# Optimization experiments

Measured on AMD Instinct MI355X. Metric: run time of the kernel, lower is better.

## Reference

```python
import jax, jax.numpy as jnp
import numpy as np


def setup_inputs() -> dict:
    key = jax.random.key(0)
    k0, k1, k2, k3, k4 = jax.random.split(key, 5)
    B, H, W, C = 8, 64, 64, 256
    d = C // 8
    scale = 0.02
    return {
        "inputs": jax.random.normal(k0, (B, H, W, C), dtype=jnp.float32),
        "w_q": jax.random.normal(k1, (C, d), dtype=jnp.float32) * scale,
        "w_k": jax.random.normal(k2, (C, d), dtype=jnp.float32) * scale,
        "w_v": jax.random.normal(k3, (C, C), dtype=jnp.float32) * scale,
        "w_out": jax.random.normal(k4, (C, C), dtype=jnp.float32) * scale,
    }


def reference(inputs, w_q, w_k, w_v, w_out):
    B, H, W, C = inputs.shape
    N = H * W
    x = inputs.reshape(B, N, C)  # 1x1 conv == per-pixel channel matmul
    q = jnp.einsum("bnc,cd->bnd", x, w_q)   # [B, N, C//8]
    k = jnp.einsum("bnc,cd->bnd", x, w_k)   # [B, N, C//8]
    v = jnp.einsum("bnc,ce->bne", x, w_v)   # [B, N, C]
    attn = jax.nn.softmax(jnp.einsum("bnd,bmd->bnm", q, k), axis=-1)  # [B, N, N]
    attended = jnp.einsum("bnm,bme->bne", attn, v)  # [B, N, C]
    out = jnp.einsum("bne,ec->bnc", attended, w_out)
    return inputs + out.reshape(B, H, W, C)
```

## Files before the change

kernel.cpp:

```cpp
#include <hip/hip_runtime.h>
#include <hip/hip_bf16.h>
#include <stdint.h>

typedef __attribute__((ext_vector_type(8))) short short8;
typedef __attribute__((ext_vector_type(8))) unsigned short ushort8;
typedef __attribute__((ext_vector_type(4))) unsigned short ushort4v;
typedef __attribute__((ext_vector_type(4))) unsigned u32x4;
typedef __attribute__((ext_vector_type(2))) float f32x2;
typedef __attribute__((ext_vector_type(4))) float f32x4;
typedef __attribute__((ext_vector_type(16))) float f32x16;

#define B_ 8
#define N_ 4096
#define C_ 256
#define D_ 32
#define LOG2E 1.44269504088896f

__device__ inline unsigned short f2bf(float f) {
  union { float f; unsigned u; } v; v.f = f;
  unsigned r = v.u + 0x7fffu + ((v.u >> 16) & 1u);
  return (unsigned short)(r >> 16);
}
__device__ inline float bf2f(unsigned short u) {
  return __uint_as_float(((unsigned)u) << 16);
}
__device__ inline float exp2_fast(float x) {
  float r; asm("v_exp_f32 %0, %1" : "=v"(r) : "v"(x)); return r;
}
__device__ inline unsigned cvt_pk_bf16(float lo, float hi) {
  unsigned r; asm("v_cvt_pk_bf16_f32 %0, %1, %2" : "=v"(r) : "v"(lo), "v"(hi)); return r;
}
__device__ inline void permlane32_swap(unsigned& a, unsigned& b) {
  asm volatile("v_permlane32_swap_b32 %0, %1" : "+v"(a), "+v"(b));
}
__device__ inline void gll16(const unsigned short* src, void* lds) {
  __builtin_amdgcn_global_load_lds((const __attribute__((address_space(1))) void*)src,
                                   (__attribute__((address_space(3))) void*)lds, 16, 0, 0);
}

__device__ inline size_t wf_addr(int C, int kk) {
  int ct = C >> 4, cl = C & 15, s = kk >> 5, gf = (kk >> 3) & 3, j = kk & 7;
  return ((size_t)((ct * 8 + s) * 64 + gf * 16 + cl)) * 8 + j;
}

__global__ __launch_bounds__(256) void prep_kernel(const float* __restrict__ wq,
                                                   const float* __restrict__ wk,
                                                   const float* __restrict__ wo,
                                                   const float* __restrict__ wv,
                                                   unsigned short* __restrict__ wf,
                                                   unsigned short* __restrict__ wv_b,
                                                   unsigned short* __restrict__ woT_b) {
  int i = blockIdx.x * 256 + threadIdx.x;
  if (i < 16384) {
    int C = i >> 8, kk = i & 255;
    float v = (C < 32) ? wq[kk * 32 + C] * LOG2E : wk[kk * 32 + (C - 32)];
    wf[wf_addr(C, kk)] = f2bf(v);
  } else if (i < 81920) {
    int j = i - 16384;
    wv_b[j] = f2bf(wv[j]);
  } else {
    int j = i - 81920;
    int e2 = j >> 8, e = j & 255;
    woT_b[j] = f2bf(wo[e * 256 + e2]);
  }
}

__global__ __launch_bounds__(256) void prep2_kernel(const unsigned short* __restrict__ woT_b,
                                                    const unsigned short* __restrict__ wv_b,
                                                    unsigned short* __restrict__ wf) {
  const int lane = threadIdx.x & 63, w = threadIdx.x >> 6;
  const int g = lane >> 4, li = lane & 15;
  const int m0 = blockIdx.x * 64 + w * 16;
  const unsigned short* arow = woT_b + (size_t)(m0 + li) * 256 + (g << 3);
  const unsigned short* brow = wv_b + (size_t)li * 256 + (g << 3);
  f32x4 acc[16] = {};
  for (int kk = 0; kk < 256; kk += 32) {
    short8 a = *reinterpret_cast<const short8*>(arow + kk);
#pragma unroll
    for (int ct = 0; ct < 16; ++ct) {
      short8 bb = *reinterpret_cast<const short8*>(brow + (size_t)ct * 16 * 256 + kk);
      acc[ct] = __builtin_amdgcn_mfma_f32_16x16x32_bf16(a, bb, acc[ct], 0, 0, 0);
    }
  }
#pragma unroll
  for (int ct = 0; ct < 16; ++ct)
#pragma unroll
    for (int r = 0; r < 4; ++r) {
      const int C = 64 + m0 + (g << 2) + r;
      const int kk = ct * 16 + li;
      wf[wf_addr(C, kk)] = f2bf(acc[ct][r]);
    }
}

__global__ __launch_bounds__(256, 2) void qkv_kernel(const float* __restrict__ x,
                                                     const unsigned short* __restrict__ wf,
                                                     unsigned short* __restrict__ q,
                                                     unsigned short* __restrict__ k,
                                                     unsigned short* __restrict__ vwT) {
  __shared__ __align__(16) unsigned short xs[64 * 256];
  const int tid = threadIdx.x;
  const int l = tid & 63, w = tid >> 6;
  const int bx = blockIdx.x;
  const int g = l >> 4, li = l & 15;
  const int m0 = bx * 64;

  const unsigned short* wfb = wf + (size_t)(w * 5) * 4096;

  short8 BA[5], BB[5];
#pragma unroll
  for (int c = 0; c < 5; ++c)
    BA[c] = *reinterpret_cast<const short8*>(wfb + ((size_t)(c * 8 + 0) * 64 + l) * 8);
#pragma unroll
  for (int c = 0; c < 5; ++c)
    BB[c] = *reinterpret_cast<const short8*>(wfb + ((size_t)(c * 8 + 1) * 64 + l) * 8);

  {
    const int row = tid >> 2, qtr = tid & 3;
    const float* src = x + (size_t)(m0 + row) * 256 + qtr * 64;
    unsigned short* dstrow = xs + row * 256;
#pragma unroll
    for (int jj = 0; jj < 8; ++jj) {
      f32x4 a0 = *reinterpret_cast<const f32x4*>(src + jj * 8);
      f32x4 a1 = *reinterpret_cast<const f32x4*>(src + jj * 8 + 4);
      union { unsigned u[4]; ushort8 v; } P;
      P.u[0] = cvt_pk_bf16(a0[0], a0[1]); P.u[1] = cvt_pk_bf16(a0[2], a0[3]);
      P.u[2] = cvt_pk_bf16(a1[0], a1[1]); P.u[3] = cvt_pk_bf16(a1[2], a1[3]);
      const int blk = (qtr * 8 + jj) ^ (row & 7);
      *reinterpret_cast<ushort8*>(dstrow + blk * 8) = P.v;
    }
  }
  __syncthreads();

  f32x4 acc[4][5] = {};

#define QSTEP(S, BV, WN, PREF)                                                       \
  {                                                                                  \
    asm volatile("s_waitcnt vmcnt(" WN ")" ::: "memory");                            \
    __builtin_amdgcn_sched_barrier(0);                                               \
    short8 a_[4];                                                                    \
    _Pragma("unroll") for (int mt = 0; mt < 4; ++mt) {                               \
      const int row = mt * 16 + li;                                                  \
      a_[mt] = *reinterpret_cast<const short8*>(                                     \
          xs + row * 256 + ((((S) * 4 + g) ^ (row & 7)) << 3));                      \
    }                                                                                \
    _Pragma("unroll") for (int mt = 0; mt < 4; ++mt)                                 \
        _Pragma("unroll") for (int c = 0; c < 5; ++c)                                \
            acc[mt][c] = __builtin_amdgcn_mfma_f32_16x16x32_bf16(a_[mt], BV[c],      \
                                                                 acc[mt][c], 0, 0, 0); \
    if (PREF) {                                                                      \
      _Pragma("unroll") for (int c = 0; c < 5; ++c)                                  \
          BV[c] = *reinterpret_cast<const short8*>(                                  \
              wfb + ((size_t)(c * 8 + (S) + 2) * 64 + l) * 8);                       \
    }                                                                                \
  }

  QSTEP(0, BA, "5", true)
  QSTEP(1, BB, "5", true)
  QSTEP(2, BA, "5", true)
  QSTEP(3, BB, "5", true)
  QSTEP(4, BA, "5", true)
  QSTEP(5, BB, "5", true)
  QSTEP(6, BA, "5", false)
  QSTEP(7, BB, "0", false)
#undef QSTEP

  const int bb_ = bx >> 6;
#pragma unroll
  for (int mt = 0; mt < 4; ++mt) {
    const int nloc = (bx & 63) * 64 + mt * 16 + (g << 2);
#pragma unroll
    for (int c = 0; c < 5; ++c) {
      const int Cg = w * 5 + c;
      if (Cg < 2) {
        const int col = Cg * 16 + li;
#pragma unroll
        for (int r = 0; r < 4; ++r)
          q[((size_t)bb_ * N_ + nloc + r) * D_ + col] = f2bf(acc[mt][c][r]);
      } else if (Cg < 4) {
        const int col = (Cg - 2) * 16 + li;
#pragma unroll
        for (int r = 0; r < 4; ++r)
          k[((size_t)bb_ * N_ + nloc + r) * D_ + col] = f2bf(acc[mt][c][r]);
      } else {
        const int vc = Cg * 16 + li - 64;
        union { unsigned u[2]; ushort4v v; } P;
        P.u[0] = cvt_pk_bf16(acc[mt][c][0], acc[mt][c][1]);
        P.u[1] = cvt_pk_bf16(acc[mt][c][2], acc[mt][c][3]);
        *reinterpret_cast<ushort4v*>(&vwT[((size_t)bb_ * C_ + vc) * N_ + nloc]) = P.v;
      }
    }
  }
}

__global__ __launch_bounds__(512, 2) void flash_kernel(const unsigned short* __restrict__ q,
                                                       const unsigned short* __restrict__ k,
                                                       const unsigned short* __restrict__ vwT,
                                                       const float* __restrict__ x,
                                                       float* __restrict__ out) {
  __shared__ __align__(16) char smem[147456];
  const int tid = threadIdx.x;
  const int l = tid & 63, w_ = tid >> 6;
  const int kvh = w_ >> 2, qg = w_ & 3;
  const int blk = blockIdx.x;
  const int b = blk & 7;
  const int qt = blk >> 3;
  const int h = l >> 5, l31 = l & 31;
  const int R = kvh * 65536;

  const unsigned short* kb_ = k + (size_t)b * N_ * D_;
  const unsigned short* vb_ = vwT + (size_t)b * C_ * N_;

  const int qposb = qt * 128 + qg * 32;
  const size_t qoff = ((size_t)b * N_ + qposb + l31) * D_ + h * 8;
  const short8 qb0 = *reinterpret_cast<const short8*>(q + qoff);
  const short8 qb1 = *reinterpret_cast<const short8*>(q + qoff + 16);
  asm volatile("s_waitcnt vmcnt(0)" ::: "memory");

  const int vrow = l >> 3;
  const int vsrc = ((l & 7) ^ ((l >> 3) & 7)) << 3;
  const int krow = l >> 2;
  const int ksrc = ((l & 3) ^ ((l >> 3) & 3)) << 3;
  const int kvbase = kvh * 2048;

#define STAGE(BUF, KV0)                                                           \
  {                                                                               \
    char* vd = smem + R + (BUF) * 32768 + qg * 8192;                              \
    _Pragma("unroll") for (int t = 0; t < 8; ++t)                                 \
        gll16(vb_ + (size_t)(qg * 64 + t * 8 + vrow) * N_ + (KV0) + vsrc,         \
              vd + t * 1024);                                                     \
    gll16(kb_ + (size_t)((KV0) + qg * 16 + krow) * D_ + ksrc,                     \
          smem + 131072 + kvh * 8192 + (BUF) * 4096 + qg * 1024);                 \
  }

  f32x16 o[8] = {};
  float lsum = 0.f;
  const f32x16 z16 = {};
  const int kkey = (l31 >> 1) & 3;

  STAGE(0, kvbase)

  for (int i = 0; i < 32; ++i) {
    const int buf = i & 1;
    asm volatile("s_waitcnt vmcnt(0)" ::: "memory");
    __builtin_amdgcn_sched_barrier(0);
    __builtin_amdgcn_s_barrier();
    if (i < 31) STAGE(buf ^ 1, kvbase + (i + 1) * 64)
    const char* Vb = smem + R + buf * 32768;
    const char* Kb = smem + 131072 + kvh * 8192 + buf * 4096;
#pragma unroll
    for (int kvt = 0; kvt < 2; ++kvt) {
      const int krow32 = (kvt * 32 + l31) * 64;
      short8 ka0 = *reinterpret_cast<const short8*>(Kb + krow32 + (((0 + h) ^ kkey) << 4));
      short8 ka1 = *reinterpret_cast<const short8*>(Kb + krow32 + (((2 + h) ^ kkey) << 4));
      f32x16 s = __builtin_amdgcn_mfma_f32_32x32x16_bf16(ka0, qb0, z16, 0, 0, 0);
      s = __builtin_amdgcn_mfma_f32_32x32x16_bf16(ka1, qb1, s, 0, 0, 0);
#pragma unroll
      for (int r = 0; r < 16; ++r) s[r] = exp2_fast(s[r]);
      lsum += (((s[0] + s[1]) + (s[2] + s[3])) + ((s[4] + s[5]) + (s[6] + s[7]))) +
              (((s[8] + s[9]) + (s[10] + s[11])) + ((s[12] + s[13]) + (s[14] + s[15])));
      short8 pf0, pf1;
      {
        unsigned x0 = cvt_pk_bf16(s[0], s[1]),   y0 = cvt_pk_bf16(s[4], s[5]);
        unsigned x1 = cvt_pk_bf16(s[2], s[3]),   y1 = cvt_pk_bf16(s[6], s[7]);
        unsigned x2 = cvt_pk_bf16(s[8], s[9]),   y2 = cvt_pk_bf16(s[12], s[13]);
        unsigned x3 = cvt_pk_bf16(s[10], s[11]), y3 = cvt_pk_bf16(s[14], s[15]);
        permlane32_swap(x0, y0); permlane32_swap(x1, y1);
        permlane32_swap(x2, y2); permlane32_swap(x3, y3);
        union U { unsigned u[4]; short8 v; };
        U u0; u0.u[0] = x0; u0.u[1] = x1; u0.u[2] = y0; u0.u[3] = y1;
        U u1; u1.u[0] = x2; u1.u[1] = x3; u1.u[2] = y2; u1.u[3] = y3;
        pf0 = u0.v; pf1 = u1.v;
      }
      __builtin_amdgcn_s_setprio(1);
#pragma unroll
      for (int ct = 0; ct < 8; ++ct) {
        const int rl = ct * 32 + l31;
        const int vkey = rl & 7;
        const int rb = rl * 128;
        short8 va0 = *reinterpret_cast<const short8*>(Vb + rb + (((kvt * 4 + 0 + h) ^ vkey) << 4));
        short8 va1 = *reinterpret_cast<const short8*>(Vb + rb + (((kvt * 4 + 2 + h) ^ vkey) << 4));
        o[ct] = __builtin_amdgcn_mfma_f32_32x32x16_bf16(va0, pf0, o[ct], 0, 0, 0);
        o[ct] = __builtin_amdgcn_mfma_f32_32x32x16_bf16(va1, pf1, o[ct], 0, 0, 0);
      }
      __builtin_amdgcn_s_setprio(0);
    }
  }

  lsum += __shfl_xor(lsum, 32);
  __syncthreads();
  float* lb = reinterpret_cast<float*>(smem + 131072);
  if (h == 0) lb[kvh * 128 + qg * 32 + l31] = lsum;
  if (kvh == 1) {
    char* ob = smem + qg * 16384;
    int pg = 0;
#pragma unroll
    for (int ct = 0; ct < 8; ++ct)
#pragma unroll
      for (int jg = 0; jg < 2; ++jg) {
        u32x4 t;
#pragma unroll
        for (int e = 0; e < 4; ++e) {
          const int j = jg * 4 + e;
          t[e] = cvt_pk_bf16(o[ct][2 * j], o[ct][2 * j + 1]);
        }
        *reinterpret_cast<u32x4*>(ob + pg * 1024 + l * 16) = t;
        ++pg;
      }
  }
  __syncthreads();
  if (kvh == 0) {
    const float inv = 1.0f / (lb[qg * 32 + l31] + lb[128 + qg * 32 + l31]);
    const char* ob = smem + qg * 16384;
    int pg = 0;
#pragma unroll
    for (int ct = 0; ct < 8; ++ct)
#pragma unroll
      for (int jg = 0; jg < 2; ++jg) {
        u32x4 t = *reinterpret_cast<const u32x4*>(ob + pg * 1024 + l * 16);
        ++pg;
#pragma unroll
        for (int e = 0; e < 4; ++e) {
          const int j = jg * 4 + e;
          o[ct][2 * j]     += bf2f((unsigned short)(t[e] & 0xffffu));
          o[ct][2 * j + 1] += bf2f((unsigned short)(t[e] >> 16));
        }
      }
    const size_t rowbase = ((size_t)b * N_ + qposb + l31) * C_;
#pragma unroll
    for (int ct = 0; ct < 8; ++ct)
#pragma unroll
      for (int j = 0; j < 8; ++j) {
        const int c = ct * 32 + 2 * (j & 1) + 8 * (j >> 1) + 4 * h;
        f32x2 xr = *reinterpret_cast<const f32x2*>(x + rowbase + c);
        f32x2 t;
        t[0] = o[ct][2 * j] * inv + xr[0];
        t[1] = o[ct][2 * j + 1] * inv + xr[1];
        *reinterpret_cast<f32x2*>(out + rowbase + c) = t;
      }
  }
#undef STAGE
}

extern "C" void kernel_launch(void* const* d_in, const int* in_sizes, int n_in,
                              void* d_out, int out_size, void* d_ws, size_t ws_size,
                              hipStream_t stream) {
  const float* x  = (const float*)d_in[0];
  const float* wq = (const float*)d_in[1];
  const float* wk = (const float*)d_in[2];
  const float* wv = (const float*)d_in[3];
  const float* wo = (const float*)d_in[4];
  float* out = (float*)d_out;
  char* ws = (char*)d_ws;
  unsigned short* wf    = (unsigned short*)(ws + 0);
  unsigned short* wv_b  = (unsigned short*)(ws + 163840);
  unsigned short* woT_b = (unsigned short*)(ws + 294912);
  unsigned short* q     = (unsigned short*)(ws + 425984);
  unsigned short* k     = (unsigned short*)(ws + 2523136);
  unsigned short* vwT   = (unsigned short*)(ws + 4620288);

  prep_kernel<<<576, 256, 0, stream>>>(wq, wk, wo, wv, wf, wv_b, woT_b);
  prep2_kernel<<<4, 256, 0, stream>>>(woT_b, wv_b, wf);
  qkv_kernel<<<512, 256, 0, stream>>>(x, wf, q, k, vwT);
  flash_kernel<<<256, 512, 0, stream>>>(q, k, vwT, x, out);
}
```

Measured before the change: 125.4 us.

## Merge weight prep kernels and halve qkv tile to raise occupancy

Folds the two weight-preparation kernels into one launch: the Wo·Wv fused-weight MFMA now reads the fp32 weights directly and converts them to bf16 inline, so the intermediate bf16 buffers and one kernel launch go away. The qkv projection kernel switches to 32-row tiles with twice as many blocks and launch bounds of 3 blocks per CU. It also issues all x loads up front into registers before converting them and storing to LDS. The aim is to cut launch overhead and improve latency hiding in the projection stage. In exchange, the prep blocks do uncoalesced strided reads of Wo, and each weight fragment in the qkv kernel is reused across fewer rows.

Result: slower. 150.0 us (+19.6%).

```diff
diff --git a/kernel.cpp b/kernel.cpp
--- a/kernel.cpp
+++ b/kernel.cpp
@@ -47,65 +47,69 @@
                                                    const float* __restrict__ wk,
                                                    const float* __restrict__ wo,
                                                    const float* __restrict__ wv,
-                                                   unsigned short* __restrict__ wf,
-                                                   unsigned short* __restrict__ wv_b,
-                                                   unsigned short* __restrict__ woT_b) {
-  int i = blockIdx.x * 256 + threadIdx.x;
-  if (i < 16384) {
+                                                   unsigned short* __restrict__ wf) {
+  const int blk = blockIdx.x;
+  if (blk < 64) {
+    int i = blk * 256 + threadIdx.x;
     int C = i >> 8, kk = i & 255;
     float v = (C < 32) ? wq[kk * 32 + C] * LOG2E : wk[kk * 32 + (C - 32)];
     wf[wf_addr(C, kk)] = f2bf(v);
-  } else if (i < 81920) {
-    int j = i - 16384;
-    wv_b[j] = f2bf(wv[j]);
   } else {
-    int j = i - 81920;
-    int e2 = j >> 8, e = j & 255;
-    woT_b[j] = f2bf(wo[e * 256 + e2]);
-  }
-}
-
-__global__ __launch_bounds__(256) void prep2_kernel(const unsigned short* __restrict__ woT_b,
-                                                    const unsigned short* __restrict__ wv_b,
-                                                    unsigned short* __restrict__ wf) {
-  const int lane = threadIdx.x & 63, w = threadIdx.x >> 6;
-  const int g = lane >> 4, li = lane & 15;
-  const int m0 = blockIdx.x * 64 + w * 16;
-  const unsigned short* arow = woT_b + (size_t)(m0 + li) * 256 + (g << 3);
-  const unsigned short* brow = wv_b + (size_t)li * 256 + (g << 3);
-  f32x4 acc[16] = {};
-  for (int kk = 0; kk < 256; kk += 32) {
-    short8 a = *reinterpret_cast<const short8*>(arow + kk);
-#pragma unroll
-    for (int ct = 0; ct < 16; ++ct) {
-      short8 bb = *reinterpret_cast<const short8*>(brow + (size_t)ct * 16 * 256 + kk);
-      acc[ct] = __builtin_amdgcn_mfma_f32_16x16x32_bf16(a, bb, acc[ct], 0, 0, 0);
+    const int lane = threadIdx.x & 63, w = threadIdx.x >> 6;
+    const int g = lane >> 4, li = lane & 15;
+    const int m0 = (blk - 64) * 64 + w * 16;
+    f32x4 acc[16] = {};
+    for (int kk = 0; kk < 256; kk += 32) {
+      short8 a;
+#pragma unroll
+      for (int e = 0; e < 8; ++e)
+        a[e] = (short)f2bf(wo[(size_t)(kk + g * 8 + e) * 256 + (m0 + li)]);
+#pragma unroll
+      for (int ct = 0; ct < 16; ++ct) {
+        const float* bsrc = wv + (size_t)(ct * 16 + li) * 256 + kk + g * 8;
+        f32x4 b0 = *reinterpret_cast<const f32x4*>(bsrc);
+        f32x4 b1 = *reinterpret_cast<const f32x4*>(bsrc + 4);
+        union { unsigned u[4]; short8 v; } Bf;
+        Bf.u[0] = cvt_pk_bf16(b0[0], b0[1]); Bf.u[1] = cvt_pk_bf16(b0[2], b0[3]);
+        Bf.u[2] = cvt_pk_bf16(b1[0], b1[1]); Bf.u[3] = cvt_pk_bf16(b1[2], b1[3]);
+        acc[ct] = __builtin_amdgcn_mfma_f32_16x16x32_bf16(a, Bf.v, acc[ct], 0, 0, 0);
+      }
     }
-  }
-#pragma unroll
-  for (int ct = 0; ct < 16; ++ct)
-#pragma unroll
-    for (int r = 0; r < 4; ++r) {
-      const int C = 64 + m0 + (g << 2) + r;
-      const int kk = ct * 16 + li;
-      wf[wf_addr(C, kk)] = f2bf(acc[ct][r]);
-    }
-}
-
-__global__ __launch_bounds__(256, 2) void qkv_kernel(const float* __restrict__ x,
+#pragma unroll
+    for (int ct = 0; ct < 16; ++ct)
+#pragma unroll
+      for (int r = 0; r < 4; ++r) {
+        const int C = 64 + m0 + (g << 2) + r;
+        const int kk = ct * 16 + li;
+        wf[wf_addr(C, kk)] = f2bf(acc[ct][r]);
+      }
+  }
+}
+
+__global__ __launch_bounds__(256, 3) void qkv_kernel(const float* __restrict__ x,
                                                      const unsigned short* __restrict__ wf,
                                                      unsigned short* __restrict__ q,
                                                      unsigned short* __restrict__ k,
                                                      unsigned short* __restrict__ vwT) {
-  __shared__ __align__(16) unsigned short xs[64 * 256];
+  __shared__ __align__(16) unsigned short xs[32 * 256];
   const int tid = threadIdx.x;
   const int l = tid & 63, w = tid >> 6;
   const int bx = blockIdx.x;
   const int g = l >> 4, li = l & 15;
-  const int m0 = bx * 64;
+  const int m0 = bx * 32;
+
+  f32x4 xf[8];
+#pragma unroll
+  for (int r2 = 0; r2 < 4; ++r2) {
+    const int idx8 = r2 * 256 + tid;
+    const int row = idx8 >> 5, xb = idx8 & 31;
+    const float* src = x + (size_t)(m0 + row) * 256 + xb * 8;
+    xf[2 * r2]     = *reinterpret_cast<const f32x4*>(src);
+    xf[2 * r2 + 1] = *reinterpret_cast<const f32x4*>(src + 4);
+  }
+  __builtin_amdgcn_sched_barrier(0);
 
   const unsigned short* wfb = wf + (size_t)(w * 5) * 4096;
-
   short8 BA[5], BB[5];
 #pragma unroll
   for (int c = 0; c < 5; ++c)
@@ -114,36 +118,32 @@
   for (int c = 0; c < 5; ++c)
     BB[c] = *reinterpret_cast<const short8*>(wfb + ((size_t)(c * 8 + 1) * 64 + l) * 8);
 
-  {
-    const int row = tid >> 2, qtr = tid & 3;
-    const float* src = x + (size_t)(m0 + row) * 256 + qtr * 64;
-    unsigned short* dstrow = xs + row * 256;
-#pragma unroll
-    for (int jj = 0; jj < 8; ++jj) {
-      f32x4 a0 = *reinterpret_cast<const f32x4*>(src + jj * 8);
-      f32x4 a1 = *reinterpret_cast<const f32x4*>(src + jj * 8 + 4);
-      union { unsigned u[4]; ushort8 v; } P;
-      P.u[0] = cvt_pk_bf16(a0[0], a0[1]); P.u[1] = cvt_pk_bf16(a0[2], a0[3]);
-      P.u[2] = cvt_pk_bf16(a1[0], a1[1]); P.u[3] = cvt_pk_bf16(a1[2], a1[3]);
-      const int blk = (qtr * 8 + jj) ^ (row & 7);
-      *reinterpret_cast<ushort8*>(dstrow + blk * 8) = P.v;
-    }
+#pragma unroll
+  for (int r2 = 0; r2 < 4; ++r2) {
+    const int idx8 = r2 * 256 + tid;
+    const int row = idx8 >> 5, xb = idx8 & 31;
+    union { unsigned u[4]; ushort8 v; } P;
+    P.u[0] = cvt_pk_bf16(xf[2 * r2][0], xf[2 * r2][1]);
+    P.u[1] = cvt_pk_bf16(xf[2 * r2][2], xf[2 * r2][3]);
+    P.u[2] = cvt_pk_bf16(xf[2 * r2 + 1][0], xf[2 * r2 + 1][1]);
+    P.u[3] = cvt_pk_bf16(xf[2 * r2 + 1][2], xf[2 * r2 + 1][3]);
+    *reinterpret_cast<ushort8*>(&xs[row * 256 + ((xb ^ (row & 7)) << 3)]) = P.v;
   }
   __syncthreads();
 
-  f32x4 acc[4][5] = {};
+  f32x4 acc[2][5] = {};
 
 #define QSTEP(S, BV, WN, PREF)                                                       \
   {                                                                                  \
     asm volatile("s_waitcnt vmcnt(" WN ")" ::: "memory");                            \
     __builtin_amdgcn_sched_barrier(0);                                               \
-    short8 a_[4];                                                                    \
-    _Pragma("unroll") for (int mt = 0; mt < 4; ++mt) {                               \
+    short8 a_[2];                                                                    \
+    _Pragma("unroll") for (int mt = 0; mt < 2; ++mt) {                               \
       const int row = mt * 16 + li;                                                  \
       a_[mt] = *reinterpret_cast<const short8*>(                                     \
           xs + row * 256 + ((((S) * 4 + g) ^ (row & 7)) << 3));                      \
     }                                                                                \
-    _Pragma("unroll") for (int mt = 0; mt < 4; ++mt)                                 \
+    _Pragma("unroll") for (int mt = 0; mt < 2; ++mt)                                 \
         _Pragma("unroll") for (int c = 0; c < 5; ++c)                                \
             acc[mt][c] = __builtin_amdgcn_mfma_f32_16x16x32_bf16(a_[mt], BV[c],      \
                                                                  acc[mt][c], 0, 0, 0); \
@@ -164,10 +164,10 @@
   QSTEP(7, BB, "0", false)
 #undef QSTEP
 
-  const int bb_ = bx >> 6;
-#pragma unroll
-  for (int mt = 0; mt < 4; ++mt) {
-    const int nloc = (bx & 63) * 64 + mt * 16 + (g << 2);
+  const int bb_ = bx >> 7;
+#pragma unroll
+  for (int mt = 0; mt < 2; ++mt) {
+    const int nloc = (bx & 127) * 32 + mt * 16 + (g << 2);
 #pragma unroll
     for (int c = 0; c < 5; ++c) {
       const int Cg = w * 5 + c;
@@ -351,15 +351,12 @@
   const float* wo = (const float*)d_in[4];
   float* out = (float*)d_out;
   char* ws = (char*)d_ws;
-  unsigned short* wf    = (unsigned short*)(ws + 0);
-  unsigned short* wv_b  = (unsigned short*)(ws + 163840);
-  unsigned short* woT_b = (unsigned short*)(ws + 294912);
-  unsigned short* q     = (unsigned short*)(ws + 425984);
-  unsigned short* k     = (unsigned short*)(ws + 2523136);
-  unsigned short* vwT   = (unsigned short*)(ws + 4620288);
-
-  prep_kernel<<<576, 256, 0, stream>>>(wq, wk, wo, wv, wf, wv_b, woT_b);
-  prep2_kernel<<<4, 256, 0, stream>>>(woT_b, wv_b, wf);
-  qkv_kernel<<<512, 256, 0, stream>>>(x, wf, q, k, vwT);
+  unsigned short* wf  = (unsigned short*)(ws + 0);
+  unsigned short* q   = (unsigned short*)(ws + 163840);
+  unsigned short* k   = (unsigned short*)(ws + 2260992);
+  unsigned short* vwT = (unsigned short*)(ws + 4358144);
+
+  prep_kernel<<<68, 256, 0, stream>>>(wq, wk, wo, wv, wf);
+  qkv_kernel<<<1024, 256, 0, stream>>>(x, wf, q, k, vwT);
   flash_kernel<<<256, 512, 0, stream>>>(q, k, vwT, x, out);
 }
```
